# Performance work log

Measured on AMD Instinct MI355X. Metric: run time of the kernel, lower is better.

Reference implementation:

```python
import jax, jax.numpy as jnp
import numpy as np

TOPK = 50
TEMPERATURE = 0.07

def _l2norm(x, eps=1e-12):
    # matches torch F.normalize: x / max(||x||, eps)
    n = jnp.sqrt(jnp.sum(x * x, axis=-1, keepdims=True))
    return x / jnp.clip(n, eps)

def setup_inputs() -> dict:
    key = jax.random.key(0)
    ks = jax.random.split(key, 16)
    B, D, C, M, V = 1024, 128, 256, 100000, 100000
    s = 1.0 / np.sqrt(D)
    s2 = 1.0 / np.sqrt(2 * D)
    sc = 1.0 / np.sqrt(C)
    return {
        "current_repr": jax.random.normal(ks[0], (B, D), jnp.float32),
        "session_ids": jax.random.randint(ks[1], (B,), 0, V),
        "item_emb": jax.random.normal(ks[2], (V, D), jnp.float32),
        "feature_queue": jax.random.normal(ks[3], (M, D), jnp.float32),
        "session_queue": jax.random.randint(ks[4], (M,), 0, V),
        "target_queue": jax.random.randint(ks[5], (M,), 0, V),
        "Wq": jax.random.normal(ks[6], (D, D), jnp.float32) * s,
        "bq": jnp.zeros((D,), jnp.float32),
        "Wk": jax.random.normal(ks[7], (D, D), jnp.float32) * s,
        "bk": jnp.zeros((D,), jnp.float32),
        "W1": jax.random.normal(ks[8], (2 * D, C), jnp.float32) * s2,
        "b1": jnp.zeros((C,), jnp.float32),
        "W2": jax.random.normal(ks[9], (C, C), jnp.float32) * sc,
        "b2": jnp.zeros((C,), jnp.float32),
        "fallback_context": jnp.zeros((D,), jnp.float32),
        "fallback_summary": jnp.zeros((C,), jnp.float32),
    }

def reference(current_repr, session_ids, item_emb, feature_queue, session_queue,
              target_queue, Wq, bq, Wk, bk, W1, b1, W2, b2,
              fallback_context, fallback_summary):
    # cosine similarity between projected queries and projected bank keys
    q = _l2norm(current_repr @ Wq + bq)            # [B, D]
    k = _l2norm(feature_queue @ Wk + bk)           # [M, D]
    sims = q @ k.T                                  # [B, M]
    # mask entries from the same session
    valid = session_queue[None, :] != session_ids[:, None]
    sims = jnp.where(valid, sims, -jnp.inf)
    top_values, top_idx = jax.lax.top_k(sims, TOPK)  # [B, K]
    sel = jnp.isfinite(top_values)
    used = jnp.any(sel, axis=1)                      # [B]
    logits = jnp.where(sel, top_values / TEMPERATURE, -1e9)
    attn = jax.nn.softmax(logits, axis=1) * sel.astype(logits.dtype)
    attn = attn / jnp.clip(jnp.sum(attn, axis=1, keepdims=True), 1e-12)
    nbr_feat = feature_queue[top_idx]                # [B, K, D]
    nbr_tgt = jnp.clip(target_queue[top_idx], 0)     # [B, K]
    context = jnp.einsum('bk,bkd->bd', attn, nbr_feat)
    tgt_emb = item_emb[nbr_tgt]                      # [B, K, D]
    h = jnp.concatenate([nbr_feat, tgt_emb], axis=-1)  # [B, K, 2D]
    h = jax.nn.gelu(h @ W1 + b1, approximate=False) @ W2 + b2  # [B, K, C]
    summary = jnp.einsum('bk,bkd->bd', attn, h)
    context = jnp.where(used[:, None], context, fallback_context[None, :])
    summary = jnp.where(used[:, None], summary, fallback_summary[None, :])
    return context, summary, used
```

## Files before the change

kernel.cpp:

```cpp
#include <hip/hip_runtime.h>
#include <hip/hip_bf16.h>

#define TOPK 50
#define CAP 512
#define MQ 100000
#define HFLOOR 0.16f
#define HBIN 0.005f

typedef float f32x4 __attribute__((ext_vector_type(4)));
typedef __bf16 bf16x8 __attribute__((ext_vector_type(8)));
typedef unsigned short u16x8 __attribute__((ext_vector_type(8)));
typedef unsigned short u16x4 __attribute__((ext_vector_type(4)));

__device__ __forceinline__ unsigned short f2bf(float f) {
    unsigned int u = __float_as_uint(f);
    return (unsigned short)((u + 0x7fffu + ((u >> 16) & 1u)) >> 16);
}

__global__ void k_transpose(const float* __restrict__ W1, const float* __restrict__ W2,
                            unsigned short* __restrict__ W1t, unsigned short* __restrict__ W2t) {
    int c = blockIdx.x & 255;
    int k = threadIdx.x;
    if (blockIdx.x < 256) W1t[c*256 + k] = f2bf(W1[k*256 + c]);
    else                  W2t[c*256 + k] = f2bf(W2[k*256 + c]);
}

__global__ void k_qproj(const float* __restrict__ cr, const float* __restrict__ Wq,
                        const float* __restrict__ bq,
                        double* __restrict__ q64, unsigned short* __restrict__ qbf) {
    int row = blockIdx.x, d = threadIdx.x;
    __shared__ double xs[128];
    __shared__ double red[128];
    xs[d] = (double)cr[row*128 + d];
    __syncthreads();
    double s = (double)bq[d];
    #pragma unroll 4
    for (int i = 0; i < 128; ++i) s += xs[i] * (double)Wq[i*128 + d];
    red[d] = s * s;
    __syncthreads();
    for (int off = 64; off > 0; off >>= 1) {
        if (d < off) red[d] += red[d + off];
        __syncthreads();
    }
    double inv = 1.0 / fmax(sqrt(red[0]), 1e-12);
    double qv = s * inv;
    q64[row*128 + d] = qv;
    qbf[row*128 + d] = f2bf((float)qv);
}

__global__ __launch_bounds__(256) void k_kproj(const float* __restrict__ fq,
        const float* __restrict__ Wk, const float* __restrict__ bk,
        unsigned short* __restrict__ k_hi, double* __restrict__ invn) {
    __shared__ __align__(16) float wks[128*128];
    __shared__ __align__(16) float fqs[128*129];
    int t = threadIdx.x;
    long row0 = (long)blockIdx.x * 128;
    for (int j = 0; j < 16; ++j) {
        int id4 = t + 256*j;
        float4 v = reinterpret_cast<const float4*>(Wk)[id4];
        *reinterpret_cast<float4*>(&wks[id4*4]) = v;
    }
    for (int j = 0; j < 16; ++j) {
        int id4 = t + 256*j;
        int r = id4 >> 5;
        int c4 = (id4 & 31) << 2;
        float4 v = {0.f, 0.f, 0.f, 0.f};
        if (row0 + r < MQ) v = *reinterpret_cast<const float4*>(&fq[(row0 + r)*128 + c4]);
        fqs[r*129 + c4 + 0] = v.x;
        fqs[r*129 + c4 + 1] = v.y;
        fqs[r*129 + c4 + 2] = v.z;
        fqs[r*129 + c4 + 3] = v.w;
    }
    __syncthreads();
    const int ct = t & 15, rt = t >> 4;
    const int r0 = rt * 8, c0 = ct * 4;
    float acc[8][8];
    #pragma unroll
    for (int a = 0; a < 8; ++a)
        #pragma unroll
        for (int b = 0; b < 8; ++b) acc[a][b] = 0.f;
    #pragma unroll 2
    for (int i = 0; i < 128; ++i) {
        float4 w0 = *reinterpret_cast<const float4*>(&wks[i*128 + c0]);
        float4 w1 = *reinterpret_cast<const float4*>(&wks[i*128 + 64 + c0]);
        float a[8];
        #pragma unroll
        for (int rr = 0; rr < 8; ++rr) a[rr] = fqs[(r0+rr)*129 + i];
        #pragma unroll
        for (int rr = 0; rr < 8; ++rr) {
            acc[rr][0] = fmaf(a[rr], w0.x, acc[rr][0]);
            acc[rr][1] = fmaf(a[rr], w0.y, acc[rr][1]);
            acc[rr][2] = fmaf(a[rr], w0.z, acc[rr][2]);
            acc[rr][3] = fmaf(a[rr], w0.w, acc[rr][3]);
            acc[rr][4] = fmaf(a[rr], w1.x, acc[rr][4]);
            acc[rr][5] = fmaf(a[rr], w1.y, acc[rr][5]);
            acc[rr][6] = fmaf(a[rr], w1.z, acc[rr][6]);
            acc[rr][7] = fmaf(a[rr], w1.w, acc[rr][7]);
        }
    }
    float bkv[8];
    #pragma unroll
    for (int cc = 0; cc < 4; ++cc) { bkv[cc] = bk[c0+cc]; bkv[4+cc] = bk[64+c0+cc]; }
    #pragma unroll
    for (int rr = 0; rr < 8; ++rr)
        #pragma unroll
        for (int cc = 0; cc < 8; ++cc) acc[rr][cc] += bkv[cc];
    __syncthreads();
    double* npart = reinterpret_cast<double*>(fqs);
    #pragma unroll
    for (int rr = 0; rr < 8; ++rr) {
        double pn = 0.0;
        #pragma unroll
        for (int cc = 0; cc < 8; ++cc) pn += (double)acc[rr][cc] * (double)acc[rr][cc];
        npart[(r0+rr)*16 + ct] = pn;
    }
    __syncthreads();
    double* invd = npart + 128*16;
    if (t < 128) {
        double nn = 0.0;
        for (int k2 = 0; k2 < 16; ++k2) nn += npart[t*16 + k2];
        double iv = 1.0 / fmax(sqrt(nn), 1e-12);
        invd[t] = iv;
        if (row0 + t < MQ) invn[row0 + t] = iv;
    }
    __syncthreads();
    #pragma unroll
    for (int rr = 0; rr < 8; ++rr) {
        long row = row0 + r0 + rr;
        if (row < MQ) {
            float iv = (float)invd[r0 + rr];
            u16x4 o0, o1;
            #pragma unroll
            for (int cc = 0; cc < 4; ++cc) {
                o0[cc] = f2bf(acc[rr][cc] * iv);
                o1[cc] = f2bf(acc[rr][4+cc] * iv);
            }
            *reinterpret_cast<u16x4*>(&k_hi[row*128 + c0]) = o0;
            *reinterpret_cast<u16x4*>(&k_hi[row*128 + 64 + c0]) = o1;
        }
    }
}

template<bool HIST>
__global__ __launch_bounds__(256) void k_sims_t(const unsigned short* __restrict__ qbf,
        const unsigned short* __restrict__ k_hi,
        int* __restrict__ rhist, const float* __restrict__ Trow,
        int* __restrict__ cnt, int* __restrict__ cand) {
    __shared__ unsigned short kt[64*128];
    int t = threadIdx.x;
    int col0 = blockIdx.x * 64;
    for (int j = 0; j < 4; ++j) {
        int chunk = t + 256*j;
        int r = chunk >> 4, s = chunk & 15;
        u16x8 v = {0,0,0,0,0,0,0,0};
        long col = col0 + r;
        if (col < MQ) v = *reinterpret_cast<const u16x8*>(&k_hi[col*128 + s*8]);
        *reinterpret_cast<u16x8*>(&kt[r*128 + s*8]) = v;
    }
    __syncthreads();
    int w = t >> 6, l = t & 63;
    int lr = l & 15, lk = l >> 4;
    bf16x8 bfr[4];
    #pragma unroll
    for (int kk = 0; kk < 4; ++kk)
        bfr[kk] = *reinterpret_cast<const bf16x8*>(&kt[(w*16 + lr)*128 + kk*32 + lk*8]);
    int colg = col0 + w*16 + lr;
    for (int rg = 0; rg < 64; ++rg) {
        const unsigned short* qrow = qbf + (rg*16 + lr)*128 + lk*8;
        f32x4 acc = {0.f, 0.f, 0.f, 0.f};
        #pragma unroll
        for (int kk = 0; kk < 4; ++kk) {
            bf16x8 a = *reinterpret_cast<const bf16x8*>(qrow + kk*32);
            acc = __builtin_amdgcn_mfma_f32_16x16x32_bf16(a, bfr[kk], acc, 0, 0, 0);
        }
        if (colg < MQ) {
            #pragma unroll
            for (int i = 0; i < 4; ++i) {
                float v = acc[i];
                int r = rg*16 + lk*4 + i;
                if (HIST) {
                    int b = (int)floorf((v - HFLOOR) * 200.0f);
                    if (b >= 0) {
                        if (b > 63) b = 63;
                        atomicAdd(&rhist[r*64 + b], 1);
                    }
                } else {
                    if (v >= Trow[r]) {
                        int pos = atomicAdd(&cnt[r], 1);
                        if (pos < CAP) cand[r*CAP + pos] = colg;
                    }
                }
            }
        }
    }
}

__global__ void k_pick(const int* __restrict__ rhist, float* __restrict__ Trow) {
    int r = blockIdx.x * 256 + threadIdx.x;
    if (r < 1024) {
        int cum = 0;
        float T = HFLOOR - HBIN;
        for (int b = 63; b >= 0; --b) {
            cum += rhist[r*64 + b];
            if (cum >= TOPK) { T = HFLOOR + HBIN * b - HBIN; break; }
        }
        Trow[r] = T;
    }
}

__global__ __launch_bounds__(256) void k_select(
        const double* __restrict__ q64, const float* __restrict__ Wk,
        const float* __restrict__ bk, const float* __restrict__ fq,
        const double* __restrict__ invn, const int* __restrict__ sq,
        const int* __restrict__ sid, const int* __restrict__ cnt,
        const int* __restrict__ cand,
        float* __restrict__ attn_g, int* __restrict__ tidx_g, int* __restrict__ used_g,
        float* __restrict__ out_ctx, float* __restrict__ out_used,
        const float* __restrict__ fb_ctx) {
    __shared__ double qs[128];
    __shared__ double wqr[128];
    __shared__ double qb_s;
    __shared__ double vals[CAP];
    __shared__ int cidx[CAP];
    __shared__ double selv[TOPK];
    __shared__ int seli[TOPK];
    __shared__ float attn_s[TOPK];
    __shared__ int used_s;
    int row = blockIdx.x, t = threadIdx.x;
    if (t < 128) qs[t] = q64[row*128 + t];
    __syncthreads();
    if (t < 128) {
        double s = 0.0;
        for (int d = 0; d < 128; ++d) s += (double)Wk[t*128 + d] * qs[d];
        wqr[t] = s;
    }
    if (t == 0) {
        double s = 0.0;
        for (int d = 0; d < 128; ++d) s += qs[d] * (double)bk[d];
        qb_s = s;
    }
    if (t < TOPK) { selv[t] = -1e290; seli[t] = 0; }
    __syncthreads();
    int n = cnt[row]; if (n > CAP) n = CAP;
    int myses = sid[row];
    for (int j = t; j < n; j += 256) {
        int c = cand[row*CAP + j];
        cidx[j] = c;
        double v;
        if (sq[c] == myses) v = -1e300;
        else {
            double s = qb_s;
            const float4* xr4 = reinterpret_cast<const float4*>(fq + (long)c*128);
            for (int i4 = 0; i4 < 32; ++i4) {
                float4 x4 = xr4[i4];
                s += (double)x4.x * wqr[i4*4+0] + (double)x4.y * wqr[i4*4+1]
                   + (double)x4.z * wqr[i4*4+2] + (double)x4.w * wqr[i4*4+3];
            }
            v = s * invn[c];
        }
        vals[j] = v;
    }
    __syncthreads();
    for (int j = t; j < n; j += 256) {
        double v = vals[j]; int ci = cidx[j];
        int rk = 0;
        for (int m2 = 0; m2 < n; ++m2) {
            double vm = vals[m2];
            rk += (vm > v) || (vm == v && cidx[m2] < ci);
        }
        if (rk < TOPK) { selv[rk] = v; seli[rk] = ci; }
    }
    __syncthreads();
    if (t == 0) {
        double vmax = -1.0e308;
        for (int r = 0; r < TOPK; ++r)
            if (selv[r] > -1e250 && selv[r] > vmax) vmax = selv[r];
        float ssum = 0.f;
        for (int r = 0; r < TOPK; ++r) {
            float ev = 0.f;
            if (selv[r] > -1e250) ev = expf((float)((selv[r] - vmax) * (1.0/0.07)));
            attn_s[r] = ev; ssum += ev;
        }
        float invs = (ssum > 0.f) ? 1.0f/ssum : 0.0f;
        for (int r = 0; r < TOPK; ++r) attn_s[r] *= invs;
        used_s = (ssum > 0.f) ? 1 : 0;
        used_g[row] = used_s;
    }
    __syncthreads();
    int used = used_s;
    if (t < TOPK) { attn_g[row*TOPK + t] = attn_s[t]; tidx_g[row*TOPK + t] = seli[t]; }
    if (t < 128) {
        float cacc = 0.f;
        for (int r = 0; r < TOPK; ++r) cacc += attn_s[r] * fq[(long)seli[r]*128 + t];
        out_ctx[row*128 + t] = used ? cacc : fb_ctx[t];
    }
    if (t == 0) out_used[row] = used ? 1.0f : 0.0f;
}

__global__ __launch_bounds__(256) void k_mlp(
        const float* __restrict__ fq, const float* __restrict__ item_emb,
        const int* __restrict__ tq,
        const unsigned short* __restrict__ W1t, const unsigned short* __restrict__ W2t,
        const float* __restrict__ b1, const float* __restrict__ b2,
        const float* __restrict__ attn_g, const int* __restrict__ tidx_g,
        const int* __restrict__ used_g,
        const float* __restrict__ fb_sum, float* __restrict__ out_sum) {
    __shared__ __align__(16) unsigned short xs[64*256];
    __shared__ float attn_s[64];
    __shared__ int tgt_s[64];
    __shared__ int tix_s[64];
    int b = blockIdx.x, t = threadIdx.x;
    if (t < 64) {
        float a = 0.f; int ti = 0;
        if (t < TOPK) { a = attn_g[b*TOPK + t]; ti = tidx_g[b*TOPK + t]; }
        attn_s[t] = a; tix_s[t] = ti;
        int tg = 0;
        if (t < TOPK) { tg = tq[ti]; if (tg < 0) tg = 0; }
        tgt_s[t] = tg;
    }
    __syncthreads();
    for (int j = 0; j < 8; ++j) {
        int chunk = t + 256*j;
        int r = chunk >> 5, s = chunk & 31;
        int sp = s ^ (r & 7);
        u16x8 o = {0,0,0,0,0,0,0,0};
        if (r < TOPK) {
            int c0 = s * 8;
            const float* src = (c0 < 128) ? (fq + (long)tix_s[r]*128 + c0)
                                          : (item_emb + (long)tgt_s[r]*128 + (c0 - 128));
            float4 v0 = *reinterpret_cast<const float4*>(src);
            float4 v1 = *reinterpret_cast<const float4*>(src + 4);
            o[0] = f2bf(v0.x); o[1] = f2bf(v0.y); o[2] = f2bf(v0.z); o[3] = f2bf(v0.w);
            o[4] = f2bf(v1.x); o[5] = f2bf(v1.y); o[6] = f2bf(v1.z); o[7] = f2bf(v1.w);
        }
        *reinterpret_cast<u16x8*>(&xs[(r*32 + sp)*8]) = o;
    }
    __syncthreads();
    int w = t >> 6, l = t & 63, lr = l & 15, lk = l >> 4;
    int wbase = w * 64;
    f32x4 zero4 = {0.f, 0.f, 0.f, 0.f};
    f32x4 acc[4][4];
    #pragma unroll
    for (int rt = 0; rt < 4; ++rt)
        #pragma unroll
        for (int ctl = 0; ctl < 4; ++ctl) acc[rt][ctl] = zero4;
    #pragma unroll
    for (int kk = 0; kk < 8; ++kk) {
        bf16x8 av[4];
        #pragma unroll
        for (int rt = 0; rt < 4; ++rt) {
            int r = rt*16 + lr;
            int sp = (kk*4 + lk) ^ (r & 7);
            av[rt] = *reinterpret_cast<const bf16x8*>(&xs[(r*32 + sp)*8]);
        }
        #pragma unroll
        for (int ctl = 0; ctl < 4; ++ctl) {
            int col = wbase + ctl*16 + lr;
            bf16x8 bv = *reinterpret_cast<const bf16x8*>(&W1t[(long)col*256 + kk*32 + lk*8]);
            #pragma unroll
            for (int rt = 0; rt < 4; ++rt)
                acc[rt][ctl] = __builtin_amdgcn_mfma_f32_16x16x32_bf16(av[rt], bv, acc[rt][ctl], 0, 0, 0);
        }
    }
    __syncthreads();
    #pragma unroll
    for (int ctl = 0; ctl < 4; ++ctl) {
        int col = wbase + ctl*16 + lr;
        float b1v = b1[col];
        #pragma unroll
        for (int rt = 0; rt < 4; ++rt) {
            #pragma unroll
            for (int i = 0; i < 4; ++i) {
                int r = rt*16 + lk*4 + i;
                float v = acc[rt][ctl][i] + b1v;
                float g = 0.5f * v * (1.0f + erff(v * 0.70710678118654752f));
                int cchunk = (col >> 3) ^ (r & 7);
                xs[(r*32 + cchunk)*8 + (col & 7)] = f2bf(g);
            }
        }
    }
    __syncthreads();
    f32x4 acc2[4][4];
    #pragma unroll
    for (int rt = 0; rt < 4; ++rt)
        #pragma unroll
        for (int ctl = 0; ctl < 4; ++ctl) acc2[rt][ctl] = zero4;
    #pragma unroll
    for (int kk = 0; kk < 8; ++kk) {
        bf16x8 av[4];
        #pragma unroll
        for (int rt = 0; rt < 4; ++rt) {
            int r = rt*16 + lr;
            int sp = (kk*4 + lk) ^ (r & 7);
            av[rt] = *reinterpret_cast<const bf16x8*>(&xs[(r*32 + sp)*8]);
        }
        #pragma unroll
        for (int ctl = 0; ctl < 4; ++ctl) {
            int col = wbase + ctl*16 + lr;
            bf16x8 bv = *reinterpret_cast<const bf16x8*>(&W2t[(long)col*256 + kk*32 + lk*8]);
            #pragma unroll
            for (int rt = 0; rt < 4; ++rt)
                acc2[rt][ctl] = __builtin_amdgcn_mfma_f32_16x16x32_bf16(av[rt], bv, acc2[rt][ctl], 0, 0, 0);
        }
    }
    int used = used_g[b];
    #pragma unroll
    for (int ctl = 0; ctl < 4; ++ctl) {
        float ps = 0.f;
        #pragma unroll
        for (int rt = 0; rt < 4; ++rt)
            #pragma unroll
            for (int i = 0; i < 4; ++i)
                ps += attn_s[rt*16 + lk*4 + i] * acc2[rt][ctl][i];
        ps += __shfl_xor(ps, 16, 64);
        ps += __shfl_xor(ps, 32, 64);
        if (l < 16) {
            int col = wbase + ctl*16 + l;
            out_sum[b*256 + col] = used ? (ps + b2[col]) : fb_sum[col];
        }
    }
}

extern "C" void kernel_launch(void* const* d_in, const int* in_sizes, int n_in,
                              void* d_out, int out_size, void* d_ws, size_t ws_size,
                              hipStream_t stream) {
    const float* cr   = (const float*)d_in[0];
    const int*   sid  = (const int*)d_in[1];
    const float* item = (const float*)d_in[2];
    const float* fq   = (const float*)d_in[3];
    const int*   sq   = (const int*)d_in[4];
    const int*   tq   = (const int*)d_in[5];
    const float* Wq   = (const float*)d_in[6];
    const float* bq   = (const float*)d_in[7];
    const float* Wk   = (const float*)d_in[8];
    const float* bk   = (const float*)d_in[9];
    const float* W1   = (const float*)d_in[10];
    const float* b1   = (const float*)d_in[11];
    const float* W2   = (const float*)d_in[12];
    const float* b2   = (const float*)d_in[13];
    const float* fbc  = (const float*)d_in[14];
    const float* fbs  = (const float*)d_in[15];

    float* out_ctx  = (float*)d_out;
    float* out_sum  = out_ctx + 1024*128;
    float* out_used = out_sum + 1024*256;

    char* w = (char*)d_ws;
    unsigned short* k_hi = (unsigned short*)w;  w += (size_t)MQ*128*2;
    double* invn = (double*)w;                  w += (size_t)MQ*8;
    double* q64 = (double*)w;                   w += (size_t)1024*128*8;
    unsigned short* qbf = (unsigned short*)w;   w += (size_t)1024*128*2;
    unsigned short* W1t = (unsigned short*)w;   w += (size_t)256*256*2;
    unsigned short* W2t = (unsigned short*)w;   w += (size_t)256*256*2;
    int* cand = (int*)w;                        w += (size_t)1024*CAP*4;
    int* cnt = (int*)w;                         w += (size_t)1024*4;
    float* attn_g = (float*)w;                  w += (size_t)1024*TOPK*4;
    int* tidx_g = (int*)w;                      w += (size_t)1024*TOPK*4;
    int* used_g = (int*)w;                      w += (size_t)1024*4;
    int* rhist = (int*)w;                       w += (size_t)1024*64*4;
    float* Trow = (float*)w;                    w += (size_t)1024*4;

    hipMemsetAsync(cnt, 0, 1024*4, stream);
    hipMemsetAsync(rhist, 0, 1024*64*4, stream);
    k_transpose<<<512, 256, 0, stream>>>(W1, W2, W1t, W2t);
    k_qproj<<<1024, 128, 0, stream>>>(cr, Wq, bq, q64, qbf);
    k_kproj<<<(MQ + 127)/128, 256, 0, stream>>>(fq, Wk, bk, k_hi, invn);
    k_sims_t<true><<<(MQ + 63)/64, 256, 0, stream>>>(qbf, k_hi, rhist, nullptr, nullptr, nullptr);
    k_pick<<<4, 256, 0, stream>>>(rhist, Trow);
    k_sims_t<false><<<(MQ + 63)/64, 256, 0, stream>>>(qbf, k_hi, nullptr, Trow, cnt, cand);
    k_select<<<1024, 256, 0, stream>>>(q64, Wk, bk, fq, invn, sq, sid, cnt, cand,
                                       attn_g, tidx_g, used_g, out_ctx, out_used, fbc);
    k_mlp<<<1024, 256, 0, stream>>>(fq, item, tq, W1t, W2t, b1, b2,
                                    attn_g, tidx_g, used_g, fbs, out_sum);
}
```

Baseline: 896.8 us.

## Replace histogram threshold pass with sampled mean/std threshold and fallback fix kernel

The full histogram sims pass, with its per-element atomics, is replaced by a sampled statistics kernel. It computes per-row mean and variance over every 8th key column and sets the threshold at mu + 2.9 sigma. The append pass now handles 256 columns per block with register-held key fragments and skips tiles whose maximum is below the threshold. It also counts confident non-same-session hits. A new per-row fix kernel runs an exact histogram fallback when too few or too many candidates are found, which guards correctness at the cost of a slow scalar path whenever the statistical threshold misses.

```diff
diff --git a/kernel.cpp b/kernel.cpp
--- a/kernel.cpp
+++ b/kernel.cpp
@@ -4,8 +4,11 @@
 #define TOPK 50
 #define CAP 512
 #define MQ 100000
-#define HFLOOR 0.16f
-#define HBIN 0.005f
+#define ZCUT 2.9f
+#define EPS2 0.006f
+#define NS_BLK 49
+#define NS_CNT 12500.0f
+#define NAPP ((MQ + 255) / 256)
 
 typedef float f32x4 __attribute__((ext_vector_type(4)));
 typedef __bf16 bf16x8 __attribute__((ext_vector_type(8)));
@@ -15,6 +18,9 @@
 __device__ __forceinline__ unsigned short f2bf(float f) {
     unsigned int u = __float_as_uint(f);
     return (unsigned short)((u + 0x7fffu + ((u >> 16) & 1u)) >> 16);
+}
+__device__ __forceinline__ float bf2f(unsigned short u) {
+    return __uint_as_float(((unsigned int)u) << 16);
 }
 
 __global__ void k_transpose(const float* __restrict__ W1, const float* __restrict__ W2,
@@ -141,53 +147,128 @@
     }
 }
 
-template<bool HIST>
-__global__ __launch_bounds__(256) void k_sims_t(const unsigned short* __restrict__ qbf,
-        const unsigned short* __restrict__ k_hi,
-        int* __restrict__ rhist, const float* __restrict__ Trow,
-        int* __restrict__ cnt, int* __restrict__ cand) {
-    __shared__ unsigned short kt[64*128];
+__global__ __launch_bounds__(256) void k_stats(const unsigned short* __restrict__ qbf,
+        const unsigned short* __restrict__ k_hi, float* __restrict__ ws_s) {
+    __shared__ float lds_s[4][1024][2];
     int t = threadIdx.x;
-    int col0 = blockIdx.x * 64;
-    for (int j = 0; j < 4; ++j) {
-        int chunk = t + 256*j;
-        int r = chunk >> 4, s = chunk & 15;
-        u16x8 v = {0,0,0,0,0,0,0,0};
-        long col = col0 + r;
-        if (col < MQ) v = *reinterpret_cast<const u16x8*>(&k_hi[col*128 + s*8]);
-        *reinterpret_cast<u16x8*>(&kt[r*128 + s*8]) = v;
-    }
-    __syncthreads();
+    int n = blockIdx.x;
     int w = t >> 6, l = t & 63;
     int lr = l & 15, lk = l >> 4;
-    bf16x8 bfr[4];
-    #pragma unroll
-    for (int kk = 0; kk < 4; ++kk)
-        bfr[kk] = *reinterpret_cast<const bf16x8*>(&kt[(w*16 + lr)*128 + kk*32 + lk*8]);
-    int colg = col0 + w*16 + lr;
+    for (int i = t; i < 4*1024*2; i += 256) ((float*)lds_s)[i] = 0.f;
+    bf16x8 bfr[4][4];
+    #pragma unroll
+    for (int cf = 0; cf < 4; ++cf) {
+        long scol = 8L * (n*256 + w*64 + cf*16 + lr);
+        #pragma unroll
+        for (int kk = 0; kk < 4; ++kk) {
+            u16x8 v = {0,0,0,0,0,0,0,0};
+            if (scol < MQ) v = *reinterpret_cast<const u16x8*>(&k_hi[scol*128 + kk*32 + lk*8]);
+            bfr[cf][kk] = *reinterpret_cast<bf16x8*>(&v);
+        }
+    }
+    __syncthreads();
     for (int rg = 0; rg < 64; ++rg) {
-        const unsigned short* qrow = qbf + (rg*16 + lr)*128 + lk*8;
-        f32x4 acc = {0.f, 0.f, 0.f, 0.f};
+        bf16x8 a[4];
+        #pragma unroll
+        for (int kk = 0; kk < 4; ++kk)
+            a[kk] = *reinterpret_cast<const bf16x8*>(&qbf[(rg*16 + lr)*128 + kk*32 + lk*8]);
+        f32x4 acc[4];
+        #pragma unroll
+        for (int cf = 0; cf < 4; ++cf) {
+            acc[cf] = (f32x4){0.f,0.f,0.f,0.f};
+            #pragma unroll
+            for (int kk = 0; kk < 4; ++kk)
+                acc[cf] = __builtin_amdgcn_mfma_f32_16x16x32_bf16(a[kk], bfr[cf][kk], acc[cf], 0, 0, 0);
+        }
+        #pragma unroll
+        for (int i = 0; i < 4; ++i) {
+            float s1 = acc[0][i] + acc[1][i] + acc[2][i] + acc[3][i];
+            float s2 = acc[0][i]*acc[0][i] + acc[1][i]*acc[1][i]
+                     + acc[2][i]*acc[2][i] + acc[3][i]*acc[3][i];
+            #pragma unroll
+            for (int m = 1; m < 16; m <<= 1) {
+                s1 += __shfl_xor(s1, m, 64);
+                s2 += __shfl_xor(s2, m, 64);
+            }
+            if (lr == 0) {
+                int row = rg*16 + lk*4 + i;
+                lds_s[w][row][0] += s1;
+                lds_s[w][row][1] += s2;
+            }
+        }
+    }
+    __syncthreads();
+    for (int r = t; r < 1024; r += 256) {
+        float a = lds_s[0][r][0] + lds_s[1][r][0] + lds_s[2][r][0] + lds_s[3][r][0];
+        float b = lds_s[0][r][1] + lds_s[1][r][1] + lds_s[2][r][1] + lds_s[3][r][1];
+        ws_s[n*2048 + r*2 + 0] = a;
+        ws_s[n*2048 + r*2 + 1] = b;
+    }
+}
+
+__global__ void k_thresh(const float* __restrict__ ws_s, float* __restrict__ Trow) {
+    int r = blockIdx.x * 256 + threadIdx.x;
+    if (r >= 1024) return;
+    float s1 = 0.f, s2 = 0.f;
+    for (int n = 0; n < NS_BLK; ++n) {
+        s1 += ws_s[n*2048 + r*2 + 0];
+        s2 += ws_s[n*2048 + r*2 + 1];
+    }
+    float mu = s1 / NS_CNT;
+    float var = s2 / NS_CNT - mu*mu;
+    float sg = sqrtf(fmaxf(var, 1e-12f));
+    Trow[r] = mu + ZCUT * sg;
+}
+
+__global__ __launch_bounds__(256) void k_append(const unsigned short* __restrict__ qbf,
+        const unsigned short* __restrict__ k_hi, const float* __restrict__ Trow,
+        const int* __restrict__ sq, const int* __restrict__ sid,
+        int* __restrict__ cnt, int* __restrict__ cnthi, int* __restrict__ cand) {
+    int t = threadIdx.x;
+    int col0 = blockIdx.x * 256;
+    int w = t >> 6, l = t & 63;
+    int lr = l & 15, lk = l >> 4;
+    bf16x8 bfr[4][4];
+    int colg[4];
+    #pragma unroll
+    for (int cf = 0; cf < 4; ++cf) {
+        long c = col0 + w*64 + cf*16 + lr;
+        colg[cf] = (int)c;
         #pragma unroll
         for (int kk = 0; kk < 4; ++kk) {
-            bf16x8 a = *reinterpret_cast<const bf16x8*>(qrow + kk*32);
-            acc = __builtin_amdgcn_mfma_f32_16x16x32_bf16(a, bfr[kk], acc, 0, 0, 0);
-        }
-        if (colg < MQ) {
-            #pragma unroll
-            for (int i = 0; i < 4; ++i) {
-                float v = acc[i];
-                int r = rg*16 + lk*4 + i;
-                if (HIST) {
-                    int b = (int)floorf((v - HFLOOR) * 200.0f);
-                    if (b >= 0) {
-                        if (b > 63) b = 63;
-                        atomicAdd(&rhist[r*64 + b], 1);
-                    }
-                } else {
-                    if (v >= Trow[r]) {
+            u16x8 v = {0,0,0,0,0,0,0,0};
+            if (c < MQ) v = *reinterpret_cast<const u16x8*>(&k_hi[c*128 + kk*32 + lk*8]);
+            bfr[cf][kk] = *reinterpret_cast<bf16x8*>(&v);
+        }
+    }
+    for (int rg = 0; rg < 64; ++rg) {
+        bf16x8 a[4];
+        #pragma unroll
+        for (int kk = 0; kk < 4; ++kk)
+            a[kk] = *reinterpret_cast<const bf16x8*>(&qbf[(rg*16 + lr)*128 + kk*32 + lk*8]);
+        f32x4 T4 = *reinterpret_cast<const f32x4*>(&Trow[rg*16 + lk*4]);
+        float Tmin = fminf(fminf(T4[0], T4[1]), fminf(T4[2], T4[3]));
+        f32x4 acc[4];
+        #pragma unroll
+        for (int cf = 0; cf < 4; ++cf) {
+            acc[cf] = (f32x4){0.f,0.f,0.f,0.f};
+            #pragma unroll
+            for (int kk = 0; kk < 4; ++kk)
+                acc[cf] = __builtin_amdgcn_mfma_f32_16x16x32_bf16(a[kk], bfr[cf][kk], acc[cf], 0, 0, 0);
+        }
+        #pragma unroll
+        for (int cf = 0; cf < 4; ++cf) {
+            float mx = fmaxf(fmaxf(acc[cf][0], acc[cf][1]), fmaxf(acc[cf][2], acc[cf][3]));
+            if (mx >= Tmin && colg[cf] < MQ) {
+                #pragma unroll
+                for (int i = 0; i < 4; ++i) {
+                    float v = acc[cf][i];
+                    if (v >= T4[i]) {
+                        int r = rg*16 + lk*4 + i;
                         int pos = atomicAdd(&cnt[r], 1);
-                        if (pos < CAP) cand[r*CAP + pos] = colg;
+                        if (pos < CAP) cand[r*CAP + pos] = colg[cf];
+                        if (v >= T4[i] + EPS2 && sq[colg[cf]] != sid[r])
+                            atomicAdd(&cnthi[r], 1);
                     }
                 }
             }
@@ -195,16 +276,57 @@
     }
 }
 
-__global__ void k_pick(const int* __restrict__ rhist, float* __restrict__ Trow) {
-    int r = blockIdx.x * 256 + threadIdx.x;
-    if (r < 1024) {
-        int cum = 0;
-        float T = HFLOOR - HBIN;
-        for (int b = 63; b >= 0; --b) {
-            cum += rhist[r*64 + b];
-            if (cum >= TOPK) { T = HFLOOR + HBIN * b - HBIN; break; }
-        }
-        Trow[r] = T;
+__global__ __launch_bounds__(256) void k_fix(const unsigned short* __restrict__ qbf,
+        const unsigned short* __restrict__ k_hi,
+        const int* __restrict__ sq, const int* __restrict__ sid,
+        int* __restrict__ cnt, const int* __restrict__ cnthi, int* __restrict__ cand) {
+    int row = blockIdx.x;
+    if (cnthi[row] >= TOPK && cnt[row] <= CAP) return;
+    __shared__ float qr[128];
+    __shared__ int hist[1024];
+    __shared__ float Tsh;
+    int t = threadIdx.x;
+    if (t < 128) qr[t] = bf2f(qbf[row*128 + t]);
+    for (int i = t; i < 1024; i += 256) hist[i] = 0;
+    __syncthreads();
+    int myses = sid[row];
+    for (int c = t; c < MQ; c += 256) {
+        if (sq[c] == myses) continue;
+        const u16x8* kr = reinterpret_cast<const u16x8*>(k_hi + (long)c*128);
+        float v = 0.f;
+        for (int j = 0; j < 16; ++j) {
+            u16x8 kv = kr[j];
+            #pragma unroll
+            for (int e = 0; e < 8; ++e) v += qr[j*8+e] * bf2f(kv[e]);
+        }
+        int b = (int)((v + 1.0f) * 512.0f);
+        b = b < 0 ? 0 : (b > 1023 ? 1023 : b);
+        atomicAdd(&hist[b], 1);
+    }
+    __syncthreads();
+    if (t == 0) {
+        int cum = 0; float T = -2.0f;
+        for (int b = 1023; b >= 0; --b) {
+            cum += hist[b];
+            if (cum >= TOPK) { T = (float)b * (1.0f/512.0f) - 1.0f - 0.005f; break; }
+        }
+        Tsh = T;
+        cnt[row] = 0;
+    }
+    __syncthreads();
+    float T = Tsh;
+    for (int c = t; c < MQ; c += 256) {
+        const u16x8* kr = reinterpret_cast<const u16x8*>(k_hi + (long)c*128);
+        float v = 0.f;
+        for (int j = 0; j < 16; ++j) {
+            u16x8 kv = kr[j];
+            #pragma unroll
+            for (int e = 0; e < 8; ++e) v += qr[j*8+e] * bf2f(kv[e]);
+        }
+        if (v >= T) {
+            int pos = atomicAdd(&cnt[row], 1);
+            if (pos < CAP) cand[row*CAP + pos] = c;
+        }
     }
 }
 
@@ -454,20 +576,22 @@
     unsigned short* W2t = (unsigned short*)w;   w += (size_t)256*256*2;
     int* cand = (int*)w;                        w += (size_t)1024*CAP*4;
     int* cnt = (int*)w;                         w += (size_t)1024*4;
+    int* cnthi = (int*)w;                       w += (size_t)1024*4;
     float* attn_g = (float*)w;                  w += (size_t)1024*TOPK*4;
     int* tidx_g = (int*)w;                      w += (size_t)1024*TOPK*4;
     int* used_g = (int*)w;                      w += (size_t)1024*4;
-    int* rhist = (int*)w;                       w += (size_t)1024*64*4;
+    float* ws_s = (float*)w;                    w += (size_t)NS_BLK*2048*4;
     float* Trow = (float*)w;                    w += (size_t)1024*4;
 
     hipMemsetAsync(cnt, 0, 1024*4, stream);
-    hipMemsetAsync(rhist, 0, 1024*64*4, stream);
+    hipMemsetAsync(cnthi, 0, 1024*4, stream);
     k_transpose<<<512, 256, 0, stream>>>(W1, W2, W1t, W2t);
     k_qproj<<<1024, 128, 0, stream>>>(cr, Wq, bq, q64, qbf);
     k_kproj<<<(MQ + 127)/128, 256, 0, stream>>>(fq, Wk, bk, k_hi, invn);
-    k_sims_t<true><<<(MQ + 63)/64, 256, 0, stream>>>(qbf, k_hi, rhist, nullptr, nullptr, nullptr);
-    k_pick<<<4, 256, 0, stream>>>(rhist, Trow);
-    k_sims_t<false><<<(MQ + 63)/64, 256, 0, stream>>>(qbf, k_hi, nullptr, Trow, cnt, cand);
+    k_stats<<<NS_BLK, 256, 0, stream>>>(qbf, k_hi, ws_s);
+    k_thresh<<<4, 256, 0, stream>>>(ws_s, Trow);
+    k_append<<<NAPP, 256, 0, stream>>>(qbf, k_hi, Trow, sq, sid, cnt, cnthi, cand);
+    k_fix<<<1024, 256, 0, stream>>>(qbf, k_hi, sq, sid, cnt, cnthi, cand);
     k_select<<<1024, 256, 0, stream>>>(q64, Wk, bk, fq, invn, sq, sid, cnt, cand,
                                        attn_g, tidx_g, used_g, out_ctx, out_used, fbc);
     k_mlp<<<1024, 256, 0, stream>>>(fq, item, tq, W1t, W2t, b1, b2,
```

New measurement: 754.1 us. -15.9%, faster.
